# Kernel optimization log

Hardware: AMD Instinct MI355X
Metric: run time of the kernel (lower is better)

The kernel has to match this reference:

```python
import jax, jax.numpy as jnp
import numpy as np

D = 64  # hidden_dim


def _bn(x, gamma, beta):
    # eval-mode BatchNorm1d with running_mean=0, running_var=1 (fresh model)
    return gamma * x + beta


def _edge_conv(h, W, b, gamma, beta):
    # h: [B,N,D]; W: [2D,D] split into Wi (acts on x_i) and Wj (acts on x_j)
    Wi, Wj = W[:D], W[D:]
    ti = jnp.einsum('bnd,de->bne', h, Wi)  # [B,N,D] (i term)
    tj = jnp.einsum('bmd,de->bme', h, Wj)  # [B,N,D] (j term)
    # e[b,i,j,:] = x_i@Wi + x_j@Wj + b  -> relu -> BN -> max over j
    e = ti[:, :, None, :] + tj[:, None, :, :] + b  # [B,N,N,D]
    e = _bn(jax.nn.relu(e), gamma, beta)
    return e.max(axis=2)  # [B,N,D]


def setup_inputs() -> dict:
    key = jax.random.key(0)
    ks = jax.random.split(key, 16)
    s = lambda k, shp, sc: (jax.random.normal(k, shp, dtype=jnp.float32) * sc)
    inp = {
        'x': s(ks[0], (32, 256, 4), 1.0),
        'W1': s(ks[1], (4, D), 0.5), 'b1': s(ks[2], (D,), 0.1),
        'g1': 1.0 + s(ks[3], (D,), 0.1), 'beta1': s(ks[4], (D,), 0.1),
        'We1': s(ks[5], (2 * D, D), 0.1), 'be1': s(ks[6], (D,), 0.1),
        'ge1': 1.0 + s(ks[7], (D,), 0.1), 'betae1': s(ks[8], (D,), 0.1),
        'We2': s(ks[9], (2 * D, D), 0.1), 'be2': s(ks[10], (D,), 0.1),
        'ge2': 1.0 + s(ks[11], (D,), 0.1), 'betae2': s(ks[12], (D,), 0.1),
        'Wg1': s(ks[13], (2 * D, D), 0.1), 'bg1': s(ks[14], (D,), 0.1),
        'Wg2': s(ks[15], (D, 2), 0.1), 'bg2': jnp.zeros((2,), jnp.float32),
    }
    return inp


def reference(x, W1, b1, g1, beta1, We1, be1, ge1, betae1, We2, be2, ge2, betae2, Wg1, bg1, Wg2, bg2):
    # input MLP: Linear -> ReLU -> BN (eval)
    h = _bn(jax.nn.relu(x @ W1 + b1), g1, beta1)  # [B,N,D]
    h = _edge_conv(h, We1, be1, ge1, betae1)
    h = _edge_conv(h, We2, be2, ge2, betae2)
    x_mean = h.mean(axis=1)  # [B,D]
    x_max = h.max(axis=1)    # [B,D]
    xg = jnp.concatenate([x_mean, x_max], axis=-1)  # [B,2D]
    # global MLP (dropout is identity in eval)
    out = jax.nn.relu(xg @ Wg1 + bg1) @ Wg2 + bg2  # [B,2]
    return out
```

## Files before the change

kernel.cpp:

```cpp
#include <hip/hip_runtime.h>

#define NB 32
#define NN 256
#define DD 64
#define SROW 68
#define FMAXV 3.402823466e+38f


__device__ __forceinline__ void conv_matvec(
    const float* Hs, int l, int d0, const float* __restrict__ We,
    float ti[4][4], float tj[4][4])
{
#pragma unroll
    for (int cc = 0; cc < 4; ++cc)
#pragma unroll
        for (int j = 0; j < 4; ++j) { ti[cc][j] = 0.f; tj[cc][j] = 0.f; }

    const float* hr0 = Hs + (size_t)(0 * 64 + l) * SROW;
    const float* hr1 = Hs + (size_t)(1 * 64 + l) * SROW;
    const float* hr2 = Hs + (size_t)(2 * 64 + l) * SROW;
    const float* hr3 = Hs + (size_t)(3 * 64 + l) * SROW;

#pragma unroll
    for (int k4 = 0; k4 < 16; ++k4) {
        float4 h0 = *(const float4*)(hr0 + k4 * 4);
        float4 h1 = *(const float4*)(hr1 + k4 * 4);
        float4 h2 = *(const float4*)(hr2 + k4 * 4);
        float4 h3 = *(const float4*)(hr3 + k4 * 4);
        const float ha[4][4] = {{h0.x, h0.y, h0.z, h0.w},
                                {h1.x, h1.y, h1.z, h1.w},
                                {h2.x, h2.y, h2.z, h2.w},
                                {h3.x, h3.y, h3.z, h3.w}};
#pragma unroll
        for (int kk = 0; kk < 4; ++kk) {
            const int k = k4 * 4 + kk;
            float4 wi = *(const float4*)(We + k * DD + d0);
            float4 wj = *(const float4*)(We + (DD + k) * DD + d0);
            const float wiv[4] = {wi.x, wi.y, wi.z, wi.w};
            const float wjv[4] = {wj.x, wj.y, wj.z, wj.w};
#pragma unroll
            for (int cc = 0; cc < 4; ++cc) {
#pragma unroll
                for (int j = 0; j < 4; ++j) {
                    ti[cc][j] = fmaf(ha[cc][kk], wiv[j], ti[cc][j]);
                    tj[cc][j] = fmaf(ha[cc][kk], wjv[j], tj[cc][j]);
                }
            }
        }
    }
}

__device__ __forceinline__ void reduce_minmax(const float tj[4][4],
                                              float rmax[4], float rmin[4])
{
    float mx[4], mn[4];
#pragma unroll
    for (int j = 0; j < 4; ++j) {
        mx[j] = fmaxf(fmaxf(tj[0][j], tj[1][j]), fmaxf(tj[2][j], tj[3][j]));
        mn[j] = fminf(fminf(tj[0][j], tj[1][j]), fminf(tj[2][j], tj[3][j]));
    }
#pragma unroll
    for (int m = 1; m < 64; m <<= 1) {
#pragma unroll
        for (int j = 0; j < 4; ++j) {
            mx[j] = fmaxf(mx[j], __shfl_xor(mx[j], m, 64));
            mn[j] = fminf(mn[j], __shfl_xor(mn[j], m, 64));
        }
    }
#pragma unroll
    for (int j = 0; j < 4; ++j) { rmax[j] = mx[j]; rmin[j] = mn[j]; }
}

__global__ __launch_bounds__(1024, 4) void k_all(
    const float* __restrict__ x,
    const float* __restrict__ W1,  const float* __restrict__ b1,
    const float* __restrict__ g1,  const float* __restrict__ beta1,
    const float* __restrict__ We1, const float* __restrict__ be1,
    const float* __restrict__ ge1, const float* __restrict__ bte1,
    const float* __restrict__ We2, const float* __restrict__ be2,
    const float* __restrict__ ge2, const float* __restrict__ bte2,
    const float* __restrict__ Wg1, const float* __restrict__ bg1,
    const float* __restrict__ Wg2, const float* __restrict__ bg2,
    float* __restrict__ out)
{
    __shared__ __align__(16) float Hs[NN * SROW];
    __shared__ float xg[2 * DD];
    __shared__ float hid[DD];

    const int b  = blockIdx.x;
    const int l  = threadIdx.x & 63;
    const int w  = __builtin_amdgcn_readfirstlane(threadIdx.x >> 6);
    const int d0 = w * 4;

#pragma unroll
    for (int cc = 0; cc < 4; ++cc) {
        const int n = cc * 64 + l;
        float4 xv = *(const float4*)(x + ((size_t)b * NN + n) * 4);
        float a[4];
#pragma unroll
        for (int j = 0; j < 4; ++j) a[j] = b1[d0 + j];
#pragma unroll
        for (int j = 0; j < 4; ++j) a[j] = fmaf(xv.x, W1[0 * DD + d0 + j], a[j]);
#pragma unroll
        for (int j = 0; j < 4; ++j) a[j] = fmaf(xv.y, W1[1 * DD + d0 + j], a[j]);
#pragma unroll
        for (int j = 0; j < 4; ++j) a[j] = fmaf(xv.z, W1[2 * DD + d0 + j], a[j]);
#pragma unroll
        for (int j = 0; j < 4; ++j) a[j] = fmaf(xv.w, W1[3 * DD + d0 + j], a[j]);
        float h[4];
#pragma unroll
        for (int j = 0; j < 4; ++j) h[j] = g1[d0 + j] * fmaxf(a[j], 0.f) + beta1[d0 + j];
        *(float4*)(Hs + (size_t)n * SROW + d0) = make_float4(h[0], h[1], h[2], h[3]);
    }
    __syncthreads();

    float ti[4][4], tj[4][4];
    float rmax[4], rmin[4];

    conv_matvec(Hs, l, d0, We1, ti, tj);
    reduce_minmax(tj, rmax, rmin);
    __syncthreads();

#pragma unroll
    for (int cc = 0; cc < 4; ++cc) {
        const int n = cc * 64 + l;
        float h[4];
#pragma unroll
        for (int j = 0; j < 4; ++j) {
            float gv = ge1[d0 + j];
            float sv = ti[cc][j] + (gv >= 0.f ? rmax[j] : rmin[j]) + be1[d0 + j];
            h[j] = gv * fmaxf(sv, 0.f) + bte1[d0 + j];
        }
        *(float4*)(Hs + (size_t)n * SROW + d0) = make_float4(h[0], h[1], h[2], h[3]);
    }
    __syncthreads();

    conv_matvec(Hs, l, d0, We2, ti, tj);
    reduce_minmax(tj, rmax, rmin);

    {
        float sm[4]  = {0.f, 0.f, 0.f, 0.f};
        float mxp[4] = {-FMAXV, -FMAXV, -FMAXV, -FMAXV};
#pragma unroll
        for (int cc = 0; cc < 4; ++cc) {
#pragma unroll
            for (int j = 0; j < 4; ++j) {
                float gv = ge2[d0 + j];
                float sv = ti[cc][j] + (gv >= 0.f ? rmax[j] : rmin[j]) + be2[d0 + j];
                float hv = gv * fmaxf(sv, 0.f) + bte2[d0 + j];
                sm[j]  += hv;
                mxp[j]  = fmaxf(mxp[j], hv);
            }
        }
#pragma unroll
        for (int m = 1; m < 64; m <<= 1) {
#pragma unroll
            for (int j = 0; j < 4; ++j) {
                sm[j]  += __shfl_xor(sm[j], m, 64);
                mxp[j]  = fmaxf(mxp[j], __shfl_xor(mxp[j], m, 64));
            }
        }
        float ssm = sm[0], smxp = mxp[0];
#pragma unroll
        for (int j = 1; j < 4; ++j) {
            ssm  = (l == j) ? sm[j]  : ssm;
            smxp = (l == j) ? mxp[j] : smxp;
        }
        if (l < 4) {
            xg[d0 + l]      = ssm * (1.f / 256.f);
            xg[DD + d0 + l] = smxp;
        }
    }
    __syncthreads();

    const int t = threadIdx.x;
    if (t < DD) {
        float a = bg1[t];
#pragma unroll
        for (int k = 0; k < 2 * DD; ++k) a = fmaf(xg[k], Wg1[k * DD + t], a);
        hid[t] = fmaxf(a, 0.f);
    }
    __syncthreads();
    if (t < 2) {
        float o = bg2[t];
#pragma unroll
        for (int j = 0; j < DD; ++j) o = fmaf(hid[j], Wg2[j * 2 + t], o);
        out[b * 2 + t] = o;
    }
}

extern "C" void kernel_launch(void* const* d_in, const int* in_sizes, int n_in,
                              void* d_out, int out_size, void* d_ws, size_t ws_size,
                              hipStream_t stream) {
    const float* x     = (const float*)d_in[0];
    const float* W1    = (const float*)d_in[1];
    const float* b1    = (const float*)d_in[2];
    const float* g1    = (const float*)d_in[3];
    const float* beta1 = (const float*)d_in[4];
    const float* We1   = (const float*)d_in[5];
    const float* be1   = (const float*)d_in[6];
    const float* ge1   = (const float*)d_in[7];
    const float* bte1  = (const float*)d_in[8];
    const float* We2   = (const float*)d_in[9];
    const float* be2   = (const float*)d_in[10];
    const float* ge2   = (const float*)d_in[11];
    const float* bte2  = (const float*)d_in[12];
    const float* Wg1   = (const float*)d_in[13];
    const float* bg1   = (const float*)d_in[14];
    const float* Wg2   = (const float*)d_in[15];
    const float* bg2   = (const float*)d_in[16];

    k_all<<<dim3(NB), dim3(1024), 0, stream>>>(
        x, W1, b1, g1, beta1,
        We1, be1, ge1, bte1,
        We2, be2, ge2, bte2,
        Wg1, bg1, Wg2, bg2, (float*)d_out);
}
```

Before: 131.6 us.

## Remap conv work so each thread computes one point over sixteen output channels

Each wave previously held four output channels for all 256 points. Now the 16 waves are split into 4 point-groups by 4 channel-groups, and each thread computes one point's 16 channels. Every hidden value read from shared memory is reused across 16 channels, and the weight loads become wave-uniform float4 reads. The max and min over points, and the final mean and max pooling, move from 64-lane shuffle trees to a padded shared-memory transpose with small partial reductions across waves. This costs several extra barriers and shared-memory round trips, and raises register use, which may hurt under the 1024-thread launch bound.

```diff
diff --git a/kernel.cpp b/kernel.cpp
--- a/kernel.cpp
+++ b/kernel.cpp
@@ -4,71 +4,45 @@
 #define NN 256
 #define DD 64
 #define SROW 68
+#define TPAD 17
 #define FMAXV 3.402823466e+38f
 
 
-__device__ __forceinline__ void conv_matvec(
-    const float* Hs, int l, int d0, const float* __restrict__ We,
-    float ti[4][4], float tj[4][4])
+__device__ __forceinline__ void conv_full(
+    const float* Hs, int n, int d0, const float* __restrict__ We,
+    float ti[16], float tj[16])
 {
 #pragma unroll
-    for (int cc = 0; cc < 4; ++cc)
-#pragma unroll
-        for (int j = 0; j < 4; ++j) { ti[cc][j] = 0.f; tj[cc][j] = 0.f; }
-
-    const float* hr0 = Hs + (size_t)(0 * 64 + l) * SROW;
-    const float* hr1 = Hs + (size_t)(1 * 64 + l) * SROW;
-    const float* hr2 = Hs + (size_t)(2 * 64 + l) * SROW;
-    const float* hr3 = Hs + (size_t)(3 * 64 + l) * SROW;
-
-#pragma unroll
-    for (int k4 = 0; k4 < 16; ++k4) {
-        float4 h0 = *(const float4*)(hr0 + k4 * 4);
-        float4 h1 = *(const float4*)(hr1 + k4 * 4);
-        float4 h2 = *(const float4*)(hr2 + k4 * 4);
-        float4 h3 = *(const float4*)(hr3 + k4 * 4);
-        const float ha[4][4] = {{h0.x, h0.y, h0.z, h0.w},
-                                {h1.x, h1.y, h1.z, h1.w},
-                                {h2.x, h2.y, h2.z, h2.w},
-                                {h3.x, h3.y, h3.z, h3.w}};
-#pragma unroll
-        for (int kk = 0; kk < 4; ++kk) {
-            const int k = k4 * 4 + kk;
-            float4 wi = *(const float4*)(We + k * DD + d0);
-            float4 wj = *(const float4*)(We + (DD + k) * DD + d0);
-            const float wiv[4] = {wi.x, wi.y, wi.z, wi.w};
-            const float wjv[4] = {wj.x, wj.y, wj.z, wj.w};
-#pragma unroll
-            for (int cc = 0; cc < 4; ++cc) {
-#pragma unroll
-                for (int j = 0; j < 4; ++j) {
-                    ti[cc][j] = fmaf(ha[cc][kk], wiv[j], ti[cc][j]);
-                    tj[cc][j] = fmaf(ha[cc][kk], wjv[j], tj[cc][j]);
-                }
-            }
-        }
-    }
-}
-
-__device__ __forceinline__ void reduce_minmax(const float tj[4][4],
-                                              float rmax[4], float rmin[4])
-{
-    float mx[4], mn[4];
-#pragma unroll
-    for (int j = 0; j < 4; ++j) {
-        mx[j] = fmaxf(fmaxf(tj[0][j], tj[1][j]), fmaxf(tj[2][j], tj[3][j]));
-        mn[j] = fminf(fminf(tj[0][j], tj[1][j]), fminf(tj[2][j], tj[3][j]));
-    }
-#pragma unroll
-    for (int m = 1; m < 64; m <<= 1) {
-#pragma unroll
-        for (int j = 0; j < 4; ++j) {
-            mx[j] = fmaxf(mx[j], __shfl_xor(mx[j], m, 64));
-            mn[j] = fminf(mn[j], __shfl_xor(mn[j], m, 64));
-        }
-    }
-#pragma unroll
-    for (int j = 0; j < 4; ++j) { rmax[j] = mx[j]; rmin[j] = mn[j]; }
+    for (int j = 0; j < 16; ++j) { ti[j] = 0.f; tj[j] = 0.f; }
+    const float* hrow = Hs + (size_t)n * SROW;
+#pragma unroll 1
+    for (int kc = 0; kc < 4; ++kc) {
+        float h[16];
+#pragma unroll
+        for (int q = 0; q < 4; ++q) {
+            float4 hv = *(const float4*)(hrow + kc * 16 + 4 * q);
+            h[4*q+0] = hv.x; h[4*q+1] = hv.y; h[4*q+2] = hv.z; h[4*q+3] = hv.w;
+        }
+#pragma unroll
+        for (int kk = 0; kk < 16; ++kk) {
+            const float hk = h[kk];
+            const float* wi = We + (size_t)(kc * 16 + kk) * DD + d0;
+            const float* wj = We + (size_t)(DD + kc * 16 + kk) * DD + d0;
+#pragma unroll
+            for (int q = 0; q < 4; ++q) {
+                float4 a = *(const float4*)(wi + 4 * q);
+                float4 c = *(const float4*)(wj + 4 * q);
+                ti[4*q+0] = fmaf(hk, a.x, ti[4*q+0]);
+                ti[4*q+1] = fmaf(hk, a.y, ti[4*q+1]);
+                ti[4*q+2] = fmaf(hk, a.z, ti[4*q+2]);
+                ti[4*q+3] = fmaf(hk, a.w, ti[4*q+3]);
+                tj[4*q+0] = fmaf(hk, c.x, tj[4*q+0]);
+                tj[4*q+1] = fmaf(hk, c.y, tj[4*q+1]);
+                tj[4*q+2] = fmaf(hk, c.z, tj[4*q+2]);
+                tj[4*q+3] = fmaf(hk, c.w, tj[4*q+3]);
+            }
+        }
+    }
 }
 
 __global__ __launch_bounds__(1024, 4) void k_all(
@@ -84,96 +58,177 @@
     float* __restrict__ out)
 {
     __shared__ __align__(16) float Hs[NN * SROW];
-    __shared__ float xg[2 * DD];
-    __shared__ float hid[DD];
-
-    const int b  = blockIdx.x;
-    const int l  = threadIdx.x & 63;
-    const int w  = __builtin_amdgcn_readfirstlane(threadIdx.x >> 6);
-    const int d0 = w * 4;
-
-#pragma unroll
-    for (int cc = 0; cc < 4; ++cc) {
-        const int n = cc * 64 + l;
+    __shared__ __align__(16) float PTmax[4][DD], PTmin[4][DD];
+    __shared__ __align__(16) float RM[DD], RMn[DD];
+    __shared__ __align__(16) float PS[4][DD], PM[4][DD];
+    __shared__ __align__(16) float xg[2 * DD];
+    __shared__ __align__(16) float hid[DD];
+
+    const int b   = blockIdx.x;
+    const int l   = threadIdx.x & 63;
+    const int w   = __builtin_amdgcn_readfirstlane(threadIdx.x >> 6);
+    const int ng  = w >> 2;
+    const int d0  = (w & 3) * 16;
+    const int n   = ng * 64 + l;
+    const int jd  = l >> 2;
+    const int cq  = l & 3;
+    float* Ts     = Hs + w * (64 * TPAD);
+
+    {
         float4 xv = *(const float4*)(x + ((size_t)b * NN + n) * 4);
-        float a[4];
-#pragma unroll
-        for (int j = 0; j < 4; ++j) a[j] = b1[d0 + j];
-#pragma unroll
-        for (int j = 0; j < 4; ++j) a[j] = fmaf(xv.x, W1[0 * DD + d0 + j], a[j]);
-#pragma unroll
-        for (int j = 0; j < 4; ++j) a[j] = fmaf(xv.y, W1[1 * DD + d0 + j], a[j]);
-#pragma unroll
-        for (int j = 0; j < 4; ++j) a[j] = fmaf(xv.z, W1[2 * DD + d0 + j], a[j]);
-#pragma unroll
-        for (int j = 0; j < 4; ++j) a[j] = fmaf(xv.w, W1[3 * DD + d0 + j], a[j]);
-        float h[4];
-#pragma unroll
-        for (int j = 0; j < 4; ++j) h[j] = g1[d0 + j] * fmaxf(a[j], 0.f) + beta1[d0 + j];
-        *(float4*)(Hs + (size_t)n * SROW + d0) = make_float4(h[0], h[1], h[2], h[3]);
-    }
-    __syncthreads();
-
-    float ti[4][4], tj[4][4];
-    float rmax[4], rmin[4];
-
-    conv_matvec(Hs, l, d0, We1, ti, tj);
-    reduce_minmax(tj, rmax, rmin);
-    __syncthreads();
-
-#pragma unroll
-    for (int cc = 0; cc < 4; ++cc) {
-        const int n = cc * 64 + l;
-        float h[4];
-#pragma unroll
-        for (int j = 0; j < 4; ++j) {
-            float gv = ge1[d0 + j];
-            float sv = ti[cc][j] + (gv >= 0.f ? rmax[j] : rmin[j]) + be1[d0 + j];
-            h[j] = gv * fmaxf(sv, 0.f) + bte1[d0 + j];
-        }
-        *(float4*)(Hs + (size_t)n * SROW + d0) = make_float4(h[0], h[1], h[2], h[3]);
-    }
-    __syncthreads();
-
-    conv_matvec(Hs, l, d0, We2, ti, tj);
-    reduce_minmax(tj, rmax, rmin);
-
-    {
-        float sm[4]  = {0.f, 0.f, 0.f, 0.f};
-        float mxp[4] = {-FMAXV, -FMAXV, -FMAXV, -FMAXV};
-#pragma unroll
-        for (int cc = 0; cc < 4; ++cc) {
-#pragma unroll
-            for (int j = 0; j < 4; ++j) {
-                float gv = ge2[d0 + j];
-                float sv = ti[cc][j] + (gv >= 0.f ? rmax[j] : rmin[j]) + be2[d0 + j];
-                float hv = gv * fmaxf(sv, 0.f) + bte2[d0 + j];
-                sm[j]  += hv;
-                mxp[j]  = fmaxf(mxp[j], hv);
-            }
-        }
-#pragma unroll
-        for (int m = 1; m < 64; m <<= 1) {
-#pragma unroll
-            for (int j = 0; j < 4; ++j) {
-                sm[j]  += __shfl_xor(sm[j], m, 64);
-                mxp[j]  = fmaxf(mxp[j], __shfl_xor(mxp[j], m, 64));
-            }
-        }
-        float ssm = sm[0], smxp = mxp[0];
-#pragma unroll
-        for (int j = 1; j < 4; ++j) {
-            ssm  = (l == j) ? sm[j]  : ssm;
-            smxp = (l == j) ? mxp[j] : smxp;
-        }
-        if (l < 4) {
-            xg[d0 + l]      = ssm * (1.f / 256.f);
-            xg[DD + d0 + l] = smxp;
-        }
+#pragma unroll
+        for (int q = 0; q < 4; ++q) {
+            float hq[4];
+#pragma unroll
+            for (int u = 0; u < 4; ++u) {
+                const int d = d0 + 4 * q + u;
+                float a = b1[d];
+                a = fmaf(xv.x, W1[0 * DD + d], a);
+                a = fmaf(xv.y, W1[1 * DD + d], a);
+                a = fmaf(xv.z, W1[2 * DD + d], a);
+                a = fmaf(xv.w, W1[3 * DD + d], a);
+                hq[u] = g1[d] * fmaxf(a, 0.f) + beta1[d];
+            }
+            *(float4*)(Hs + (size_t)n * SROW + d0 + 4 * q) =
+                make_float4(hq[0], hq[1], hq[2], hq[3]);
+        }
+    }
+    __syncthreads();
+
+    float ti[16], tj[16];
+
+    conv_full(Hs, n, d0, We1, ti, tj);
+    __syncthreads();
+
+#pragma unroll
+    for (int j = 0; j < 16; ++j) Ts[l * TPAD + j] = tj[j];
+    __syncthreads();
+
+    {
+        float mx = -FMAXV, mn = FMAXV;
+#pragma unroll
+        for (int r = 0; r < 16; ++r) {
+            float v = Ts[(cq * 16 + r) * TPAD + jd];
+            mx = fmaxf(mx, v); mn = fminf(mn, v);
+        }
+        mx = fmaxf(mx, __shfl_xor(mx, 1, 64));
+        mx = fmaxf(mx, __shfl_xor(mx, 2, 64));
+        mn = fminf(mn, __shfl_xor(mn, 1, 64));
+        mn = fminf(mn, __shfl_xor(mn, 2, 64));
+        if (cq == 0) { PTmax[ng][d0 + jd] = mx; PTmin[ng][d0 + jd] = mn; }
+    }
+    __syncthreads();
+
+    {
+        const int t = threadIdx.x;
+        if (t < DD)
+            RM[t] = fmaxf(fmaxf(PTmax[0][t], PTmax[1][t]),
+                          fmaxf(PTmax[2][t], PTmax[3][t]));
+        else if (t < 2 * DD) {
+            const int d = t - DD;
+            RMn[d] = fminf(fminf(PTmin[0][d], PTmin[1][d]),
+                           fminf(PTmin[2][d], PTmin[3][d]));
+        }
+    }
+    __syncthreads();
+
+    {
+#pragma unroll
+        for (int q = 0; q < 4; ++q) {
+            float4 rmx = *(const float4*)(&RM[d0 + 4 * q]);
+            float4 rmn = *(const float4*)(&RMn[d0 + 4 * q]);
+            const float rmax[4] = {rmx.x, rmx.y, rmx.z, rmx.w};
+            const float rmin[4] = {rmn.x, rmn.y, rmn.z, rmn.w};
+            float hq[4];
+#pragma unroll
+            for (int u = 0; u < 4; ++u) {
+                const int d = d0 + 4 * q + u;
+                const float gv = ge1[d];
+                const float sv = ti[4*q+u] + (gv >= 0.f ? rmax[u] : rmin[u]) + be1[d];
+                hq[u] = gv * fmaxf(sv, 0.f) + bte1[d];
+            }
+            *(float4*)(Hs + (size_t)n * SROW + d0 + 4 * q) =
+                make_float4(hq[0], hq[1], hq[2], hq[3]);
+        }
+    }
+    __syncthreads();
+
+    conv_full(Hs, n, d0, We2, ti, tj);
+    __syncthreads();
+
+#pragma unroll
+    for (int j = 0; j < 16; ++j) Ts[l * TPAD + j] = tj[j];
+    __syncthreads();
+
+    {
+        float mx = -FMAXV, mn = FMAXV;
+#pragma unroll
+        for (int r = 0; r < 16; ++r) {
+            float v = Ts[(cq * 16 + r) * TPAD + jd];
+            mx = fmaxf(mx, v); mn = fminf(mn, v);
+        }
+        mx = fmaxf(mx, __shfl_xor(mx, 1, 64));
+        mx = fmaxf(mx, __shfl_xor(mx, 2, 64));
+        mn = fminf(mn, __shfl_xor(mn, 1, 64));
+        mn = fminf(mn, __shfl_xor(mn, 2, 64));
+        if (cq == 0) { PTmax[ng][d0 + jd] = mx; PTmin[ng][d0 + jd] = mn; }
+    }
+    __syncthreads();
+
+    {
+        const int t = threadIdx.x;
+        if (t < DD)
+            RM[t] = fmaxf(fmaxf(PTmax[0][t], PTmax[1][t]),
+                          fmaxf(PTmax[2][t], PTmax[3][t]));
+        else if (t < 2 * DD) {
+            const int d = t - DD;
+            RMn[d] = fminf(fminf(PTmin[0][d], PTmin[1][d]),
+                           fminf(PTmin[2][d], PTmin[3][d]));
+        }
+    }
+    __syncthreads();
+
+    {
+#pragma unroll
+        for (int q = 0; q < 4; ++q) {
+            float4 rmx = *(const float4*)(&RM[d0 + 4 * q]);
+            float4 rmn = *(const float4*)(&RMn[d0 + 4 * q]);
+            const float rmax[4] = {rmx.x, rmx.y, rmx.z, rmx.w};
+            const float rmin[4] = {rmn.x, rmn.y, rmn.z, rmn.w};
+#pragma unroll
+            for (int u = 0; u < 4; ++u) {
+                const int d = d0 + 4 * q + u;
+                const float gv = ge2[d];
+                const float sv = ti[4*q+u] + (gv >= 0.f ? rmax[u] : rmin[u]) + be2[d];
+                Ts[l * TPAD + 4 * q + u] = gv * fmaxf(sv, 0.f) + bte2[d];
+            }
+        }
+    }
+    __syncthreads();
+
+    {
+        float s = 0.f, mx = -FMAXV;
+#pragma unroll
+        for (int r = 0; r < 16; ++r) {
+            float v = Ts[(cq * 16 + r) * TPAD + jd];
+            s += v; mx = fmaxf(mx, v);
+        }
+        s += __shfl_xor(s, 1, 64);
+        s += __shfl_xor(s, 2, 64);
+        mx = fmaxf(mx, __shfl_xor(mx, 1, 64));
+        mx = fmaxf(mx, __shfl_xor(mx, 2, 64));
+        if (cq == 0) { PS[ng][d0 + jd] = s; PM[ng][d0 + jd] = mx; }
     }
     __syncthreads();
 
     const int t = threadIdx.x;
+    if (t < DD) {
+        xg[t] = (PS[0][t] + PS[1][t] + PS[2][t] + PS[3][t]) * (1.f / 256.f);
+    } else if (t < 2 * DD) {
+        const int d = t - DD;
+        xg[t] = fmaxf(fmaxf(PM[0][d], PM[1][d]), fmaxf(PM[2][d], PM[3][d]));
+    }
+    __syncthreads();
     if (t < DD) {
         float a = bg1[t];
 #pragma unroll
```

New measurement: 117.6 us. 10.7% less time.

## Transpose shared activations and split waves between ti and tj matvecs

Applied to the files above, without the earlier changes.

Shared activations are now stored feature-major (HT[d][n]). Each wave computes either the i-term or the j-term for an 8-column slice, with every thread handling 4 consecutive points. This halves the weight loads per FMA and gives each thread a 4x8 outer-product tile fed by float4 shared reads. The j-term max/min now goes through shared arrays with an extra barrier, and half of the waves sit idle during the epilogue.

```diff
diff --git a/kernel.cpp b/kernel.cpp
--- a/kernel.cpp
+++ b/kernel.cpp
@@ -3,72 +3,31 @@
 #define NB 32
 #define NN 256
 #define DD 64
-#define SROW 68
 #define FMAXV 3.402823466e+38f
 
 
-__device__ __forceinline__ void conv_matvec(
-    const float* Hs, int l, int d0, const float* __restrict__ We,
-    float ti[4][4], float tj[4][4])
+__device__ __forceinline__ void conv_quad(
+    const float* HT, int nq, int d0, const float* __restrict__ Wb,
+    float acc[4][8])
 {
 #pragma unroll
-    for (int cc = 0; cc < 4; ++cc)
-#pragma unroll
-        for (int j = 0; j < 4; ++j) { ti[cc][j] = 0.f; tj[cc][j] = 0.f; }
-
-    const float* hr0 = Hs + (size_t)(0 * 64 + l) * SROW;
-    const float* hr1 = Hs + (size_t)(1 * 64 + l) * SROW;
-    const float* hr2 = Hs + (size_t)(2 * 64 + l) * SROW;
-    const float* hr3 = Hs + (size_t)(3 * 64 + l) * SROW;
-
-#pragma unroll
-    for (int k4 = 0; k4 < 16; ++k4) {
-        float4 h0 = *(const float4*)(hr0 + k4 * 4);
-        float4 h1 = *(const float4*)(hr1 + k4 * 4);
-        float4 h2 = *(const float4*)(hr2 + k4 * 4);
-        float4 h3 = *(const float4*)(hr3 + k4 * 4);
-        const float ha[4][4] = {{h0.x, h0.y, h0.z, h0.w},
-                                {h1.x, h1.y, h1.z, h1.w},
-                                {h2.x, h2.y, h2.z, h2.w},
-                                {h3.x, h3.y, h3.z, h3.w}};
-#pragma unroll
-        for (int kk = 0; kk < 4; ++kk) {
-            const int k = k4 * 4 + kk;
-            float4 wi = *(const float4*)(We + k * DD + d0);
-            float4 wj = *(const float4*)(We + (DD + k) * DD + d0);
-            const float wiv[4] = {wi.x, wi.y, wi.z, wi.w};
-            const float wjv[4] = {wj.x, wj.y, wj.z, wj.w};
-#pragma unroll
-            for (int cc = 0; cc < 4; ++cc) {
-#pragma unroll
-                for (int j = 0; j < 4; ++j) {
-                    ti[cc][j] = fmaf(ha[cc][kk], wiv[j], ti[cc][j]);
-                    tj[cc][j] = fmaf(ha[cc][kk], wjv[j], tj[cc][j]);
-                }
-            }
-        }
-    }
-}
-
-__device__ __forceinline__ void reduce_minmax(const float tj[4][4],
-                                              float rmax[4], float rmin[4])
-{
-    float mx[4], mn[4];
-#pragma unroll
-    for (int j = 0; j < 4; ++j) {
-        mx[j] = fmaxf(fmaxf(tj[0][j], tj[1][j]), fmaxf(tj[2][j], tj[3][j]));
-        mn[j] = fminf(fminf(tj[0][j], tj[1][j]), fminf(tj[2][j], tj[3][j]));
-    }
-#pragma unroll
-    for (int m = 1; m < 64; m <<= 1) {
-#pragma unroll
-        for (int j = 0; j < 4; ++j) {
-            mx[j] = fmaxf(mx[j], __shfl_xor(mx[j], m, 64));
-            mn[j] = fminf(mn[j], __shfl_xor(mn[j], m, 64));
-        }
-    }
-#pragma unroll
-    for (int j = 0; j < 4; ++j) { rmax[j] = mx[j]; rmin[j] = mn[j]; }
+    for (int r = 0; r < 4; ++r)
+#pragma unroll
+        for (int c = 0; c < 8; ++c) acc[r][c] = 0.f;
+    const float* hp = HT + 4 * nq;
+#pragma unroll 4
+    for (int k = 0; k < DD; ++k) {
+        float4 hv = *(const float4*)(hp + k * NN);
+        float4 w0 = *(const float4*)(Wb + k * DD + d0);
+        float4 w1 = *(const float4*)(Wb + k * DD + d0 + 4);
+        const float hr[4] = {hv.x, hv.y, hv.z, hv.w};
+        const float wv[8] = {w0.x, w0.y, w0.z, w0.w, w1.x, w1.y, w1.z, w1.w};
+#pragma unroll
+        for (int r = 0; r < 4; ++r)
+#pragma unroll
+            for (int c = 0; c < 8; ++c)
+                acc[r][c] = fmaf(hr[r], wv[c], acc[r][c]);
+    }
 }
 
 __global__ __launch_bounds__(1024, 4) void k_all(
@@ -83,97 +42,146 @@
     const float* __restrict__ Wg2, const float* __restrict__ bg2,
     float* __restrict__ out)
 {
-    __shared__ __align__(16) float Hs[NN * SROW];
-    __shared__ float xg[2 * DD];
-    __shared__ float hid[DD];
+    __shared__ __align__(16) float HT[DD * NN];
+    __shared__ float RMx[DD], RMn[DD];
+    __shared__ float xg[2 * DD], hid[DD];
 
     const int b  = blockIdx.x;
-    const int l  = threadIdx.x & 63;
-    const int w  = __builtin_amdgcn_readfirstlane(threadIdx.x >> 6);
-    const int d0 = w * 4;
-
-#pragma unroll
-    for (int cc = 0; cc < 4; ++cc) {
-        const int n = cc * 64 + l;
-        float4 xv = *(const float4*)(x + ((size_t)b * NN + n) * 4);
-        float a[4];
-#pragma unroll
-        for (int j = 0; j < 4; ++j) a[j] = b1[d0 + j];
-#pragma unroll
-        for (int j = 0; j < 4; ++j) a[j] = fmaf(xv.x, W1[0 * DD + d0 + j], a[j]);
-#pragma unroll
-        for (int j = 0; j < 4; ++j) a[j] = fmaf(xv.y, W1[1 * DD + d0 + j], a[j]);
-#pragma unroll
-        for (int j = 0; j < 4; ++j) a[j] = fmaf(xv.z, W1[2 * DD + d0 + j], a[j]);
-#pragma unroll
-        for (int j = 0; j < 4; ++j) a[j] = fmaf(xv.w, W1[3 * DD + d0 + j], a[j]);
-        float h[4];
-#pragma unroll
-        for (int j = 0; j < 4; ++j) h[j] = g1[d0 + j] * fmaxf(a[j], 0.f) + beta1[d0 + j];
-        *(float4*)(Hs + (size_t)n * SROW + d0) = make_float4(h[0], h[1], h[2], h[3]);
-    }
-    __syncthreads();
-
-    float ti[4][4], tj[4][4];
-    float rmax[4], rmin[4];
-
-    conv_matvec(Hs, l, d0, We1, ti, tj);
-    reduce_minmax(tj, rmax, rmin);
-    __syncthreads();
-
-#pragma unroll
-    for (int cc = 0; cc < 4; ++cc) {
-        const int n = cc * 64 + l;
-        float h[4];
-#pragma unroll
-        for (int j = 0; j < 4; ++j) {
-            float gv = ge1[d0 + j];
-            float sv = ti[cc][j] + (gv >= 0.f ? rmax[j] : rmin[j]) + be1[d0 + j];
-            h[j] = gv * fmaxf(sv, 0.f) + bte1[d0 + j];
-        }
-        *(float4*)(Hs + (size_t)n * SROW + d0) = make_float4(h[0], h[1], h[2], h[3]);
-    }
-    __syncthreads();
-
-    conv_matvec(Hs, l, d0, We2, ti, tj);
-    reduce_minmax(tj, rmax, rmin);
+    const int t  = threadIdx.x;
+    const int nq = t & 63;
+    const int os = __builtin_amdgcn_readfirstlane(t >> 6);
+    const bool isTi = (os < 8);
+    const int d0 = (os & 7) * 8;
 
     {
-        float sm[4]  = {0.f, 0.f, 0.f, 0.f};
-        float mxp[4] = {-FMAXV, -FMAXV, -FMAXV, -FMAXV};
-#pragma unroll
-        for (int cc = 0; cc < 4; ++cc) {
-#pragma unroll
-            for (int j = 0; j < 4; ++j) {
-                float gv = ge2[d0 + j];
-                float sv = ti[cc][j] + (gv >= 0.f ? rmax[j] : rmin[j]) + be2[d0 + j];
-                float hv = gv * fmaxf(sv, 0.f) + bte2[d0 + j];
-                sm[j]  += hv;
-                mxp[j]  = fmaxf(mxp[j], hv);
-            }
+        const int dl = os * 4;
+        float hq[4][4];
+#pragma unroll
+        for (int r = 0; r < 4; ++r) {
+            float4 xv = *(const float4*)(x + ((size_t)b * NN + 4 * nq + r) * 4);
+#pragma unroll
+            for (int u = 0; u < 4; ++u) {
+                const int d = dl + u;
+                float a = b1[d];
+                a = fmaf(xv.x, W1[0 * DD + d], a);
+                a = fmaf(xv.y, W1[1 * DD + d], a);
+                a = fmaf(xv.z, W1[2 * DD + d], a);
+                a = fmaf(xv.w, W1[3 * DD + d], a);
+                hq[u][r] = g1[d] * fmaxf(a, 0.f) + beta1[d];
+            }
+        }
+#pragma unroll
+        for (int u = 0; u < 4; ++u)
+            *(float4*)(HT + (dl + u) * NN + 4 * nq) =
+                make_float4(hq[u][0], hq[u][1], hq[u][2], hq[u][3]);
+    }
+    __syncthreads();
+
+    float acc[4][8];
+
+    conv_quad(HT, nq, d0, isTi ? We1 : (We1 + DD * DD), acc);
+    if (!isTi) {
+        float mx[8], mn[8];
+#pragma unroll
+        for (int c = 0; c < 8; ++c) {
+            mx[c] = fmaxf(fmaxf(acc[0][c], acc[1][c]), fmaxf(acc[2][c], acc[3][c]));
+            mn[c] = fminf(fminf(acc[0][c], acc[1][c]), fminf(acc[2][c], acc[3][c]));
         }
 #pragma unroll
         for (int m = 1; m < 64; m <<= 1) {
 #pragma unroll
-            for (int j = 0; j < 4; ++j) {
-                sm[j]  += __shfl_xor(sm[j], m, 64);
-                mxp[j]  = fmaxf(mxp[j], __shfl_xor(mxp[j], m, 64));
-            }
-        }
-        float ssm = sm[0], smxp = mxp[0];
-#pragma unroll
-        for (int j = 1; j < 4; ++j) {
-            ssm  = (l == j) ? sm[j]  : ssm;
-            smxp = (l == j) ? mxp[j] : smxp;
-        }
-        if (l < 4) {
-            xg[d0 + l]      = ssm * (1.f / 256.f);
-            xg[DD + d0 + l] = smxp;
-        }
-    }
-    __syncthreads();
-
-    const int t = threadIdx.x;
+            for (int c = 0; c < 8; ++c) {
+                mx[c] = fmaxf(mx[c], __shfl_xor(mx[c], m, 64));
+                mn[c] = fminf(mn[c], __shfl_xor(mn[c], m, 64));
+            }
+        }
+        float smx = mx[0], smn = mn[0];
+#pragma unroll
+        for (int c = 1; c < 8; ++c) {
+            smx = (nq == c) ? mx[c] : smx;
+            smn = (nq == c) ? mn[c] : smn;
+        }
+        if (nq < 8) { RMx[d0 + nq] = smx; RMn[d0 + nq] = smn; }
+    }
+    __syncthreads();
+
+    if (isTi) {
+#pragma unroll
+        for (int c = 0; c < 8; ++c) {
+            const int d = d0 + c;
+            const float gv = ge1[d], bv = be1[d], bt = bte1[d];
+            const float pick = (gv >= 0.f) ? RMx[d] : RMn[d];
+            float4 o;
+            o.x = gv * fmaxf(acc[0][c] + pick + bv, 0.f) + bt;
+            o.y = gv * fmaxf(acc[1][c] + pick + bv, 0.f) + bt;
+            o.z = gv * fmaxf(acc[2][c] + pick + bv, 0.f) + bt;
+            o.w = gv * fmaxf(acc[3][c] + pick + bv, 0.f) + bt;
+            *(float4*)(HT + d * NN + 4 * nq) = o;
+        }
+    }
+    __syncthreads();
+
+    conv_quad(HT, nq, d0, isTi ? We2 : (We2 + DD * DD), acc);
+    if (!isTi) {
+        float mx[8], mn[8];
+#pragma unroll
+        for (int c = 0; c < 8; ++c) {
+            mx[c] = fmaxf(fmaxf(acc[0][c], acc[1][c]), fmaxf(acc[2][c], acc[3][c]));
+            mn[c] = fminf(fminf(acc[0][c], acc[1][c]), fminf(acc[2][c], acc[3][c]));
+        }
+#pragma unroll
+        for (int m = 1; m < 64; m <<= 1) {
+#pragma unroll
+            for (int c = 0; c < 8; ++c) {
+                mx[c] = fmaxf(mx[c], __shfl_xor(mx[c], m, 64));
+                mn[c] = fminf(mn[c], __shfl_xor(mn[c], m, 64));
+            }
+        }
+        float smx = mx[0], smn = mn[0];
+#pragma unroll
+        for (int c = 1; c < 8; ++c) {
+            smx = (nq == c) ? mx[c] : smx;
+            smn = (nq == c) ? mn[c] : smn;
+        }
+        if (nq < 8) { RMx[d0 + nq] = smx; RMn[d0 + nq] = smn; }
+    }
+    __syncthreads();
+
+    if (isTi) {
+        float sm[8], mxp[8];
+#pragma unroll
+        for (int c = 0; c < 8; ++c) {
+            const int d = d0 + c;
+            const float gv = ge2[d], bv = be2[d], bt = bte2[d];
+            const float pick = (gv >= 0.f) ? RMx[d] : RMn[d];
+            const float h0 = gv * fmaxf(acc[0][c] + pick + bv, 0.f) + bt;
+            const float h1 = gv * fmaxf(acc[1][c] + pick + bv, 0.f) + bt;
+            const float h2 = gv * fmaxf(acc[2][c] + pick + bv, 0.f) + bt;
+            const float h3 = gv * fmaxf(acc[3][c] + pick + bv, 0.f) + bt;
+            sm[c]  = (h0 + h1) + (h2 + h3);
+            mxp[c] = fmaxf(fmaxf(h0, h1), fmaxf(h2, h3));
+        }
+#pragma unroll
+        for (int m = 1; m < 64; m <<= 1) {
+#pragma unroll
+            for (int c = 0; c < 8; ++c) {
+                sm[c]  += __shfl_xor(sm[c], m, 64);
+                mxp[c]  = fmaxf(mxp[c], __shfl_xor(mxp[c], m, 64));
+            }
+        }
+        float ssm = sm[0], smx = mxp[0];
+#pragma unroll
+        for (int c = 1; c < 8; ++c) {
+            ssm = (nq == c) ? sm[c]  : ssm;
+            smx = (nq == c) ? mxp[c] : smx;
+        }
+        if (nq < 8) {
+            xg[d0 + nq]      = ssm * (1.f / 256.f);
+            xg[DD + d0 + nq] = smx;
+        }
+    }
+    __syncthreads();
+
     if (t < DD) {
         float a = bg1[t];
 #pragma unroll
```

New measurement: 116.1 us. -11.8%, faster.
